# Kernel optimization log

Measured on AMD Instinct MI355X. Metric: run time of the kernel, lower is better.

The kernel has to match this reference:

```python
import jax, jax.numpy as jnp
import numpy as np

N_NODES = 100000
N_EDGES = 600000
DIM = 128          # node feature dim == hidden_dim == output_dim
NUM_HEADS = 4
HEAD_DIM = DIM // NUM_HEADS


def setup_inputs() -> dict:
    key = jax.random.key(0)
    ks = jax.random.split(key, 8)
    s = 1.0 / np.sqrt(DIM).astype(np.float32)
    nodes = jax.random.normal(ks[0], (N_NODES, DIM), jnp.float32)
    senders = jax.random.randint(ks[1], (N_EDGES,), 0, N_NODES, jnp.int32)
    receivers = jax.random.randint(ks[2], (N_EDGES,), 0, N_NODES, jnp.int32)
    Wq = jax.random.normal(ks[3], (DIM, DIM), jnp.float32) * s
    Wk = jax.random.normal(ks[4], (DIM, DIM), jnp.float32) * s
    Wv = jax.random.normal(ks[5], (DIM, DIM), jnp.float32) * s
    Wo = jax.random.normal(ks[6], (DIM, DIM), jnp.float32) * s
    bq = jnp.zeros((DIM,), jnp.float32)
    bk = jnp.zeros((DIM,), jnp.float32)
    bv = jnp.zeros((DIM,), jnp.float32)
    bo = jnp.zeros((DIM,), jnp.float32)
    return {"nodes": nodes, "senders": senders, "receivers": receivers,
            "Wq": Wq, "bq": bq, "Wk": Wk, "bk": bk,
            "Wv": Wv, "bv": bv, "Wo": Wo, "bo": bo}


def reference(nodes, senders, receivers, Wq, bq, Wk, bk, Wv, bv, Wo, bo):
    N = nodes.shape[0]
    inv_sqrt_hd = jnp.float32(1.0 / np.sqrt(HEAD_DIM))
    # Q/K/V projections, reshaped to [N, H, hd]
    q = (nodes @ Wq + bq).reshape(N, NUM_HEADS, HEAD_DIM)
    k = (nodes @ Wk + bk).reshape(N, NUM_HEADS, HEAD_DIM)
    v = (nodes @ Wv + bv).reshape(N, NUM_HEADS, HEAD_DIM)
    # Gather per edge: [E, H, hd]
    q_s = q[senders]
    k_r = k[receivers]
    scores = jnp.sum(q_s * k_r, axis=-1) * inv_sqrt_hd  # [E, H]
    # NOTE: faithful to source -- softmax is over the HEADS axis, not neighbors
    attn = jax.nn.softmax(scores, axis=-1)              # [E, H]
    weighted = (v[senders] * attn[:, :, None]).reshape(-1, DIM)  # [E, DIM]
    aggregated = jax.ops.segment_sum(weighted, receivers, num_segments=N)  # [N, DIM]
    out = aggregated @ Wo + bo
    # residual: nodes.shape[-1] == output_dim
    return out + nodes
```

## Files before the change

### kernel.cpp

```cpp
#include <hip/hip_runtime.h>
#include <hip/hip_bf16.h>

#define N_DIM 128
#define NHEADS 4
#define HEAD_DIM 32

typedef unsigned short bf16_t;
typedef short bf16x8 __attribute__((ext_vector_type(8)));
typedef float f32x4 __attribute__((ext_vector_type(4)));

__device__ __forceinline__ float bf16_to_f32(unsigned int u16) {
    union { unsigned int i; float f; } x;
    x.i = u16 << 16;
    return x.f;
}

__device__ __forceinline__ bf16_t f32_to_bf16(float f) {
    union { float f; unsigned int i; } x;
    x.f = f;
    unsigned int r = x.i + 0x7FFFu + ((x.i >> 16) & 1u);
    return (bf16_t)(r >> 16);
}

#define LDA_STRIDE 136

__global__ __launch_bounds__(128) void transpose_w_kernel(
    const float* __restrict__ Wq, const float* __restrict__ Wk,
    const float* __restrict__ Wv, const float* __restrict__ Wo,
    bf16_t* __restrict__ Wt, bf16_t* __restrict__ Wot)
{
    const int n = blockIdx.x;
    const int k = threadIdx.x;
    const float* W; bf16_t* dst; int nl;
    if (n < 128)      { W = Wq; nl = n;       dst = Wt  + n * 128; }
    else if (n < 256) { W = Wk; nl = n - 128; dst = Wt  + n * 128; }
    else if (n < 384) { W = Wv; nl = n - 256; dst = Wt  + n * 128; }
    else              { W = Wo; nl = n - 384; dst = Wot + (n - 384) * 128; }
    dst[k] = f32_to_bf16(W[k * 128 + nl]);
}

__global__ __launch_bounds__(256) void qkv_mfma_kernel(
    const float* __restrict__ nodes,
    const bf16_t* __restrict__ Wt,
    const float* __restrict__ bq, const float* __restrict__ bk,
    const float* __restrict__ bv,
    bf16_t* __restrict__ qb, bf16_t* __restrict__ kb, bf16_t* __restrict__ vb,
    int N)
{
    __shared__ bf16_t lds_a[32 * LDA_STRIDE];
    const int tid = threadIdx.x;
    const int m0 = blockIdx.x * 32;

#pragma unroll
    for (int i = 0; i < 4; ++i) {
        const int f = tid + 256 * i;
        const int row = f >> 5, c4 = f & 31;
        const int g = m0 + row;
        float4 v = make_float4(0.f, 0.f, 0.f, 0.f);
        if (g < N) v = ((const float4*)nodes)[(size_t)g * 32 + c4];
        ushort4 u;
        u.x = f32_to_bf16(v.x); u.y = f32_to_bf16(v.y);
        u.z = f32_to_bf16(v.z); u.w = f32_to_bf16(v.w);
        *(ushort4*)(lds_a + row * LDA_STRIDE + c4 * 4) = u;
    }
    __syncthreads();

    const int w  = tid >> 6;
    const int l  = tid & 63;
    const int lr = l & 15;
    const int lg = l >> 4;

    bf16x8 a[2][4];
#pragma unroll
    for (int mt = 0; mt < 2; ++mt)
#pragma unroll
        for (int kt = 0; kt < 4; ++kt)
            a[mt][kt] = *(const bf16x8*)(lds_a + (mt * 16 + lr) * LDA_STRIDE
                                         + kt * 32 + lg * 8);

#pragma unroll
    for (int ni = 0; ni < 6; ++ni) {
        const int nt = w * 6 + ni;
        const int col = nt * 16 + lr;
        f32x4 acc0 = {0.f, 0.f, 0.f, 0.f};
        f32x4 acc1 = {0.f, 0.f, 0.f, 0.f};
#pragma unroll
        for (int kt = 0; kt < 4; ++kt) {
            const bf16x8 b = *(const bf16x8*)(Wt + (size_t)col * 128
                                              + kt * 32 + lg * 8);
            acc0 = __builtin_amdgcn_mfma_f32_16x16x32_bf16(a[0][kt], b, acc0, 0, 0, 0);
            acc1 = __builtin_amdgcn_mfma_f32_16x16x32_bf16(a[1][kt], b, acc1, 0, 0, 0);
        }
        bf16_t* dst; int cl; const float* bias;
        if (nt < 8)       { dst = qb; cl = col;       bias = bq; }
        else if (nt < 16) { dst = kb; cl = col - 128; bias = bk; }
        else              { dst = vb; cl = col - 256; bias = bv; }
        const float bb = bias[cl];
#pragma unroll
        for (int j = 0; j < 4; ++j) {
            const int r0 = m0 + lg * 4 + j;
            if (r0 < N) dst[(size_t)r0 * 128 + cl] = f32_to_bf16(acc0[j] + bb);
            const int r1 = m0 + 16 + lg * 4 + j;
            if (r1 < N) dst[(size_t)r1 * 128 + cl] = f32_to_bf16(acc1[j] + bb);
        }
    }
}

__global__ __launch_bounds__(256) void hist_kernel(
    const int* __restrict__ receivers, int* __restrict__ cnt, int E)
{
    const int i = blockIdx.x * 256 + threadIdx.x;
    if (i < E) atomicAdd(&cnt[receivers[i]], 1);
}

__global__ __launch_bounds__(256) void scan_block_kernel(
    const int* __restrict__ cnt, int* __restrict__ starts,
    int* __restrict__ bsum, int N)
{
    __shared__ int sc[256];
    const int t = threadIdx.x;
    const int base = blockIdx.x * 1024 + t * 4;
    int v0 = (base + 0 < N) ? cnt[base + 0] : 0;
    int v1 = (base + 1 < N) ? cnt[base + 1] : 0;
    int v2 = (base + 2 < N) ? cnt[base + 2] : 0;
    int v3 = (base + 3 < N) ? cnt[base + 3] : 0;
    const int s = v0 + v1 + v2 + v3;
    sc[t] = s;
    __syncthreads();
    for (int off = 1; off < 256; off <<= 1) {
        int x = (t >= off) ? sc[t - off] : 0;
        __syncthreads();
        sc[t] += x;
        __syncthreads();
    }
    int excl = sc[t] - s;
    if (base + 0 < N) starts[base + 0] = excl;
    if (base + 1 < N) starts[base + 1] = excl + v0;
    if (base + 2 < N) starts[base + 2] = excl + v0 + v1;
    if (base + 3 < N) starts[base + 3] = excl + v0 + v1 + v2;
    if (t == 255) bsum[blockIdx.x] = sc[255];
}

__global__ __launch_bounds__(256) void scan_top_kernel(
    const int* __restrict__ bsum, int* __restrict__ boff,
    int* __restrict__ starts, int nb, int N)
{
    __shared__ int sc[256];
    const int t = threadIdx.x;
    const int s = (t < nb) ? bsum[t] : 0;
    sc[t] = s;
    __syncthreads();
    for (int off = 1; off < 256; off <<= 1) {
        int x = (t >= off) ? sc[t - off] : 0;
        __syncthreads();
        sc[t] += x;
        __syncthreads();
    }
    if (t < nb) boff[t] = sc[t] - s;
    if (t == 255) starts[N] = sc[255];
}

__global__ __launch_bounds__(256) void scan_add_kernel(
    int* __restrict__ starts, int* __restrict__ cursor,
    const int* __restrict__ boff, int N)
{
    const int t = threadIdx.x;
    const int base = blockIdx.x * 1024 + t * 4;
    const int o = boff[blockIdx.x];
#pragma unroll
    for (int k = 0; k < 4; ++k) {
        const int i = base + k;
        if (i < N) {
            const int v = starts[i] + o;
            starts[i] = v;
            cursor[i] = v;
        }
    }
}

__global__ __launch_bounds__(256) void scatter_kernel(
    const int* __restrict__ senders, const int* __restrict__ receivers,
    int* __restrict__ cursor, int* __restrict__ elist, int E)
{
    const int i = blockIdx.x * 256 + threadIdx.x;
    if (i < E) {
        const int pos = atomicAdd(&cursor[receivers[i]], 1);
        elist[pos] = senders[i];
    }
}

__global__ __launch_bounds__(256) void agg_kernel(
    const int* __restrict__ starts, const int* __restrict__ elist,
    const bf16_t* __restrict__ qb, const bf16_t* __restrict__ kb,
    const bf16_t* __restrict__ vb,
    bf16_t* __restrict__ agg_b, int N)
{
    const int r = blockIdx.x * 4 + (threadIdx.x >> 6);
    const int lane = threadIdx.x & 63;
    if (r >= N) return;

    const int start = starts[r];
    const int end   = starts[r + 1];
    const int c = lane * 2;

    const unsigned int ku = *(const unsigned int*)(kb + (size_t)r * N_DIM + c);
    const float kx = bf16_to_f32(ku & 0xffffu), ky = bf16_to_f32(ku >> 16);

    float ax = 0.f, ay = 0.f;
    const float scale = 0.17677669529663687f;
    const int h = lane >> 4;

    for (int j0 = start; j0 < end; j0 += 64) {
        const int ids = (j0 + lane < end) ? elist[j0 + lane] : 0;
        const int jm = min(64, end - j0);
        for (int j = 0; j < jm; ++j) {
            const int s = __shfl(ids, j);
            const unsigned int qu =
                *(const unsigned int*)(qb + (size_t)s * N_DIM + c);
            const unsigned int vu =
                *(const unsigned int*)(vb + (size_t)s * N_DIM + c);
            const float qx = bf16_to_f32(qu & 0xffffu), qy = bf16_to_f32(qu >> 16);

            float p = qx * kx + qy * ky;
            p += __shfl_xor(p, 1);
            p += __shfl_xor(p, 2);
            p += __shfl_xor(p, 4);
            p += __shfl_xor(p, 8);

            const float s0 = __shfl(p, 0)  * scale;
            const float s1 = __shfl(p, 16) * scale;
            const float s2 = __shfl(p, 32) * scale;
            const float s3 = __shfl(p, 48) * scale;

            const float m = fmaxf(fmaxf(s0, s1), fmaxf(s2, s3));
            const float e0 = __expf(s0 - m);
            const float e1 = __expf(s1 - m);
            const float e2 = __expf(s2 - m);
            const float e3 = __expf(s3 - m);
            const float inv = 1.0f / (e0 + e1 + e2 + e3);
            const float aw = (h == 0 ? e0 : h == 1 ? e1 : h == 2 ? e2 : e3) * inv;

            ax = fmaf(bf16_to_f32(vu & 0xffffu), aw, ax);
            ay = fmaf(bf16_to_f32(vu >> 16),     aw, ay);
        }
    }

    const unsigned int packed =
        (unsigned int)f32_to_bf16(ax) | ((unsigned int)f32_to_bf16(ay) << 16);
    *(unsigned int*)(agg_b + (size_t)r * N_DIM + c) = packed;
}

__global__ __launch_bounds__(256) void out_mfma_b_kernel(
    const float* __restrict__ nodes,
    const bf16_t* __restrict__ agg_b,
    const bf16_t* __restrict__ Wot,
    const float* __restrict__ bo,
    float* __restrict__ out, int N)
{
    __shared__ bf16_t lds_a[32 * LDA_STRIDE];
    const int tid = threadIdx.x;
    const int m0 = blockIdx.x * 32;

#pragma unroll
    for (int i = 0; i < 4; ++i) {
        const int f = tid + 256 * i;
        const int row = f >> 5, c4 = f & 31;
        const int g = m0 + row;
        ushort4 u = make_ushort4(0, 0, 0, 0);
        if (g < N) u = ((const ushort4*)(agg_b + (size_t)g * N_DIM))[c4];
        *(ushort4*)(lds_a + row * LDA_STRIDE + c4 * 4) = u;
    }
    __syncthreads();

    const int w  = tid >> 6;
    const int l  = tid & 63;
    const int lr = l & 15;
    const int lg = l >> 4;

    bf16x8 a[2][4];
#pragma unroll
    for (int mt = 0; mt < 2; ++mt)
#pragma unroll
        for (int kt = 0; kt < 4; ++kt)
            a[mt][kt] = *(const bf16x8*)(lds_a + (mt * 16 + lr) * LDA_STRIDE
                                         + kt * 32 + lg * 8);

#pragma unroll
    for (int ni = 0; ni < 2; ++ni) {
        const int nt = w * 2 + ni;
        const int col = nt * 16 + lr;
        f32x4 acc0 = {0.f, 0.f, 0.f, 0.f};
        f32x4 acc1 = {0.f, 0.f, 0.f, 0.f};
#pragma unroll
        for (int kt = 0; kt < 4; ++kt) {
            const bf16x8 b = *(const bf16x8*)(Wot + (size_t)col * 128
                                              + kt * 32 + lg * 8);
            acc0 = __builtin_amdgcn_mfma_f32_16x16x32_bf16(a[0][kt], b, acc0, 0, 0, 0);
            acc1 = __builtin_amdgcn_mfma_f32_16x16x32_bf16(a[1][kt], b, acc1, 0, 0, 0);
        }
        const float bb = bo[col];
#pragma unroll
        for (int j = 0; j < 4; ++j) {
            const int r0 = m0 + lg * 4 + j;
            if (r0 < N)
                out[(size_t)r0 * 128 + col] =
                    acc0[j] + bb + nodes[(size_t)r0 * 128 + col];
            const int r1 = m0 + 16 + lg * 4 + j;
            if (r1 < N)
                out[(size_t)r1 * 128 + col] =
                    acc1[j] + bb + nodes[(size_t)r1 * 128 + col];
        }
    }
}

__global__ __launch_bounds__(256) void edge_kernel(
    const int* __restrict__ senders, const int* __restrict__ receivers,
    const bf16_t* __restrict__ qb, const bf16_t* __restrict__ kb,
    const bf16_t* __restrict__ vb,
    float* __restrict__ agg, int E)
{
    const int wid = threadIdx.x >> 6;
    const int lane = threadIdx.x & 63;
    const int e = blockIdx.x * 4 + wid;
    if (e >= E) return;

    const int s = senders[e];
    const int r = receivers[e];

    const int c = lane * 2;
    const unsigned int qu = *(const unsigned int*)(qb + (size_t)s * N_DIM + c);
    const unsigned int ku = *(const unsigned int*)(kb + (size_t)r * N_DIM + c);
    const unsigned int vu = *(const unsigned int*)(vb + (size_t)s * N_DIM + c);

    const float qx = bf16_to_f32(qu & 0xffffu), qy = bf16_to_f32(qu >> 16);
    const float kx = bf16_to_f32(ku & 0xffffu), ky = bf16_to_f32(ku >> 16);

    float p = qx * kx + qy * ky;
    p += __shfl_xor(p, 1);
    p += __shfl_xor(p, 2);
    p += __shfl_xor(p, 4);
    p += __shfl_xor(p, 8);

    const float scale = 0.17677669529663687f;
    const float s0 = __shfl(p, 0)  * scale;
    const float s1 = __shfl(p, 16) * scale;
    const float s2 = __shfl(p, 32) * scale;
    const float s3 = __shfl(p, 48) * scale;

    const float m = fmaxf(fmaxf(s0, s1), fmaxf(s2, s3));
    const float e0 = __expf(s0 - m);
    const float e1 = __expf(s1 - m);
    const float e2 = __expf(s2 - m);
    const float e3 = __expf(s3 - m);
    const float inv = 1.0f / (e0 + e1 + e2 + e3);

    const int h = lane >> 4;
    const float aw = (h == 0 ? e0 : h == 1 ? e1 : h == 2 ? e2 : e3) * inv;

    const float wx = bf16_to_f32(vu & 0xffffu) * aw;
    const float wy = bf16_to_f32(vu >> 16) * aw;

    float* dst = agg + (size_t)r * N_DIM + c;
    atomicAdd(dst, wx);
    atomicAdd(dst + 1, wy);
}

__global__ __launch_bounds__(256) void out_mfma_kernel(
    const float* __restrict__ nodes,
    const bf16_t* __restrict__ Wot,
    const float* __restrict__ bo,
    float* __restrict__ out, int N)
{
    __shared__ bf16_t lds_a[32 * LDA_STRIDE];
    const int tid = threadIdx.x;
    const int m0 = blockIdx.x * 32;

#pragma unroll
    for (int i = 0; i < 4; ++i) {
        const int f = tid + 256 * i;
        const int row = f >> 5, c4 = f & 31;
        const int g = m0 + row;
        float4 v = make_float4(0.f, 0.f, 0.f, 0.f);
        if (g < N) v = ((const float4*)out)[(size_t)g * 32 + c4];
        ushort4 u;
        u.x = f32_to_bf16(v.x); u.y = f32_to_bf16(v.y);
        u.z = f32_to_bf16(v.z); u.w = f32_to_bf16(v.w);
        *(ushort4*)(lds_a + row * LDA_STRIDE + c4 * 4) = u;
    }
    __syncthreads();

    const int w  = tid >> 6;
    const int l  = tid & 63;
    const int lr = l & 15;
    const int lg = l >> 4;

    bf16x8 a[2][4];
#pragma unroll
    for (int mt = 0; mt < 2; ++mt)
#pragma unroll
        for (int kt = 0; kt < 4; ++kt)
            a[mt][kt] = *(const bf16x8*)(lds_a + (mt * 16 + lr) * LDA_STRIDE
                                         + kt * 32 + lg * 8);

#pragma unroll
    for (int ni = 0; ni < 2; ++ni) {
        const int nt = w * 2 + ni;
        const int col = nt * 16 + lr;
        f32x4 acc0 = {0.f, 0.f, 0.f, 0.f};
        f32x4 acc1 = {0.f, 0.f, 0.f, 0.f};
#pragma unroll
        for (int kt = 0; kt < 4; ++kt) {
            const bf16x8 b = *(const bf16x8*)(Wot + (size_t)col * 128
                                              + kt * 32 + lg * 8);
            acc0 = __builtin_amdgcn_mfma_f32_16x16x32_bf16(a[0][kt], b, acc0, 0, 0, 0);
            acc1 = __builtin_amdgcn_mfma_f32_16x16x32_bf16(a[1][kt], b, acc1, 0, 0, 0);
        }
        const float bb = bo[col];
#pragma unroll
        for (int j = 0; j < 4; ++j) {
            const int r0 = m0 + lg * 4 + j;
            if (r0 < N)
                out[(size_t)r0 * 128 + col] =
                    acc0[j] + bb + nodes[(size_t)r0 * 128 + col];
            const int r1 = m0 + 16 + lg * 4 + j;
            if (r1 < N)
                out[(size_t)r1 * 128 + col] =
                    acc1[j] + bb + nodes[(size_t)r1 * 128 + col];
        }
    }
}

extern "C" void kernel_launch(void* const* d_in, const int* in_sizes, int n_in,
                              void* d_out, int out_size, void* d_ws, size_t ws_size,
                              hipStream_t stream)
{
    const float* nodes   = (const float*)d_in[0];
    const int* senders   = (const int*)d_in[1];
    const int* receivers = (const int*)d_in[2];
    const float* Wq = (const float*)d_in[3];
    const float* bq = (const float*)d_in[4];
    const float* Wk = (const float*)d_in[5];
    const float* bk = (const float*)d_in[6];
    const float* Wv = (const float*)d_in[7];
    const float* bv = (const float*)d_in[8];
    const float* Wo = (const float*)d_in[9];
    const float* bo = (const float*)d_in[10];

    const int N = in_sizes[0] / N_DIM;
    const int E = in_sizes[1];

    float* out = (float*)d_out;
    char* ws = (char*)d_ws;

    const size_t row_bytes = (size_t)N * N_DIM * sizeof(bf16_t);
    size_t off = 0;
    bf16_t* qb    = (bf16_t*)(ws + off); off += row_bytes;
    bf16_t* kb    = (bf16_t*)(ws + off); off += row_bytes;
    bf16_t* vb    = (bf16_t*)(ws + off); off += row_bytes;
    bf16_t* Wt    = (bf16_t*)(ws + off); off += 384 * 128 * sizeof(bf16_t);
    bf16_t* Wot   = (bf16_t*)(ws + off); off += 128 * 128 * sizeof(bf16_t);
    bf16_t* agg_b = (bf16_t*)(ws + off); off += row_bytes;
    int* cnt      = (int*)(ws + off);    off += (size_t)N * 4;
    int* starts   = (int*)(ws + off);    off += (size_t)(N + 1) * 4;
    int* cursor   = (int*)(ws + off);    off += (size_t)N * 4;
    int* elist    = (int*)(ws + off);    off += (size_t)E * 4;
    int* bsum     = (int*)(ws + off);    off += 256 * 4;
    int* boff     = (int*)(ws + off);    off += 256 * 4;
    const size_t need_csr = off;
    const size_t need_mid = 3 * row_bytes + (384 + 128) * 128 * sizeof(bf16_t);

    const int nb = (N + 1023) / 1024;

    if (ws_size >= need_csr && nb <= 256) {
        transpose_w_kernel<<<512, 128, 0, stream>>>(Wq, Wk, Wv, Wo, Wt, Wot);
        qkv_mfma_kernel<<<(N + 31) / 32, 256, 0, stream>>>(
            nodes, Wt, bq, bk, bv, qb, kb, vb, N);

        hipMemsetAsync(cnt, 0, (size_t)N * 4, stream);
        hist_kernel<<<(E + 255) / 256, 256, 0, stream>>>(receivers, cnt, E);
        scan_block_kernel<<<nb, 256, 0, stream>>>(cnt, starts, bsum, N);
        scan_top_kernel<<<1, 256, 0, stream>>>(bsum, boff, starts, nb, N);
        scan_add_kernel<<<nb, 256, 0, stream>>>(starts, cursor, boff, N);
        scatter_kernel<<<(E + 255) / 256, 256, 0, stream>>>(
            senders, receivers, cursor, elist, E);

        agg_kernel<<<(N + 3) / 4, 256, 0, stream>>>(
            starts, elist, qb, kb, vb, agg_b, N);

        out_mfma_b_kernel<<<(N + 31) / 32, 256, 0, stream>>>(
            nodes, agg_b, Wot, bo, out, N);
    } else if (ws_size >= need_mid) {
        hipMemsetAsync(d_out, 0, (size_t)N * N_DIM * sizeof(float), stream);
        transpose_w_kernel<<<512, 128, 0, stream>>>(Wq, Wk, Wv, Wo, Wt, Wot);
        qkv_mfma_kernel<<<(N + 31) / 32, 256, 0, stream>>>(
            nodes, Wt, bq, bk, bv, qb, kb, vb, N);
        edge_kernel<<<(E + 3) / 4, 256, 0, stream>>>(
            senders, receivers, qb, kb, vb, out, E);
        out_mfma_kernel<<<(N + 31) / 32, 256, 0, stream>>>(
            nodes, Wot, bo, out, N);
    }
}
```

Measured before the change: 356.8 us.

## Precompute per-edge head softmax in separate kernel and permute weights into CSR

Moves the q·k score and head-softmax computation out of the per-receiver aggregation loop into a per-edge kernel that uses one thread per edge and writes packed bf16 attention weights. The scatter kernel now also permutes these weights into CSR order, so the aggregation only gathers v rows and weights. This removes the q gather and the cross-lane shuffle reductions from the inner loop. In exchange it adds an extra kernel with uncoalesced per-thread row reads and extra traffic for the weight buffer, and it rounds the attention weights to bf16.

```diff
diff --git a/kernel.cpp b/kernel.cpp
--- a/kernel.cpp
+++ b/kernel.cpp
@@ -13,6 +13,13 @@
     union { unsigned int i; float f; } x;
     x.i = u16 << 16;
     return x.f;
+}
+
+__device__ __forceinline__ float lof(unsigned int u) {
+    union { unsigned int i; float f; } x; x.i = u << 16; return x.f;
+}
+__device__ __forceinline__ float hif(unsigned int u) {
+    union { unsigned int i; float f; } x; x.i = u & 0xffff0000u; return x.f;
 }
 
 __device__ __forceinline__ bf16_t f32_to_bf16(float f) {
@@ -20,6 +27,12 @@
     x.f = f;
     unsigned int r = x.i + 0x7FFFu + ((x.i >> 16) & 1u);
     return (bf16_t)(r >> 16);
+}
+
+__device__ __forceinline__ float dot2(unsigned int a, unsigned int b, float acc) {
+    acc = fmaf(lof(a), lof(b), acc);
+    acc = fmaf(hif(a), hif(b), acc);
+    return acc;
 }
 
 #define LDA_STRIDE 136
@@ -104,6 +117,44 @@
             if (r1 < N) dst[(size_t)r1 * 128 + cl] = f32_to_bf16(acc1[j] + bb);
         }
     }
+}
+
+__global__ __launch_bounds__(256) void edge_attn_kernel(
+    const int* __restrict__ senders, const int* __restrict__ receivers,
+    const bf16_t* __restrict__ qb, const bf16_t* __restrict__ kb,
+    unsigned int* __restrict__ attn2, int E)
+{
+    const int e = blockIdx.x * 256 + threadIdx.x;
+    if (e >= E) return;
+    const uint4* qr = (const uint4*)(qb + (size_t)senders[e] * N_DIM);
+    const uint4* kr = (const uint4*)(kb + (size_t)receivers[e] * N_DIM);
+
+    float d[4];
+#pragma unroll
+    for (int h = 0; h < 4; ++h) {
+        float acc = 0.f;
+#pragma unroll
+        for (int i = 0; i < 4; ++i) {
+            const uint4 qu = qr[h * 4 + i];
+            const uint4 ku = kr[h * 4 + i];
+            acc = dot2(qu.x, ku.x, acc);
+            acc = dot2(qu.y, ku.y, acc);
+            acc = dot2(qu.z, ku.z, acc);
+            acc = dot2(qu.w, ku.w, acc);
+        }
+        d[h] = acc * 0.17677669529663687f;
+    }
+
+    const float m = fmaxf(fmaxf(d[0], d[1]), fmaxf(d[2], d[3]));
+    float e0 = __expf(d[0] - m), e1 = __expf(d[1] - m);
+    float e2 = __expf(d[2] - m), e3 = __expf(d[3] - m);
+    const float inv = 1.f / (e0 + e1 + e2 + e3);
+    e0 *= inv; e1 *= inv; e2 *= inv; e3 *= inv;
+
+    attn2[(size_t)e * 2 + 0] =
+        (unsigned)f32_to_bf16(e0) | ((unsigned)f32_to_bf16(e1) << 16);
+    attn2[(size_t)e * 2 + 1] =
+        (unsigned)f32_to_bf16(e2) | ((unsigned)f32_to_bf16(e3) << 16);
 }
 
 __global__ __launch_bounds__(256) void hist_kernel(
@@ -180,18 +231,21 @@
 
 __global__ __launch_bounds__(256) void scatter_kernel(
     const int* __restrict__ senders, const int* __restrict__ receivers,
-    int* __restrict__ cursor, int* __restrict__ elist, int E)
+    const unsigned int* __restrict__ attn2,
+    int* __restrict__ cursor, int* __restrict__ elist,
+    unsigned int* __restrict__ wlist2, int E)
 {
     const int i = blockIdx.x * 256 + threadIdx.x;
     if (i < E) {
         const int pos = atomicAdd(&cursor[receivers[i]], 1);
         elist[pos] = senders[i];
-    }
-}
-
-__global__ __launch_bounds__(256) void agg_kernel(
+        ((uint2*)wlist2)[pos] = ((const uint2*)attn2)[i];
+    }
+}
+
+__global__ __launch_bounds__(256) void agg2_kernel(
     const int* __restrict__ starts, const int* __restrict__ elist,
-    const bf16_t* __restrict__ qb, const bf16_t* __restrict__ kb,
+    const unsigned int* __restrict__ wlist2,
     const bf16_t* __restrict__ vb,
     bf16_t* __restrict__ agg_b, int N)
 {
@@ -202,46 +256,23 @@
     const int start = starts[r];
     const int end   = starts[r + 1];
     const int c = lane * 2;
-
-    const unsigned int ku = *(const unsigned int*)(kb + (size_t)r * N_DIM + c);
-    const float kx = bf16_to_f32(ku & 0xffffu), ky = bf16_to_f32(ku >> 16);
+    const int h = lane >> 4;
+    const int hw = h >> 1;
+    const int hs = h & 1;
 
     float ax = 0.f, ay = 0.f;
-    const float scale = 0.17677669529663687f;
-    const int h = lane >> 4;
 
     for (int j0 = start; j0 < end; j0 += 64) {
         const int ids = (j0 + lane < end) ? elist[j0 + lane] : 0;
         const int jm = min(64, end - j0);
         for (int j = 0; j < jm; ++j) {
             const int s = __shfl(ids, j);
-            const unsigned int qu =
-                *(const unsigned int*)(qb + (size_t)s * N_DIM + c);
+            const unsigned int wu = wlist2[(size_t)(j0 + j) * 2 + hw];
+            const float w = hs ? hif(wu) : lof(wu);
             const unsigned int vu =
                 *(const unsigned int*)(vb + (size_t)s * N_DIM + c);
-            const float qx = bf16_to_f32(qu & 0xffffu), qy = bf16_to_f32(qu >> 16);
-
-            float p = qx * kx + qy * ky;
-            p += __shfl_xor(p, 1);
-            p += __shfl_xor(p, 2);
-            p += __shfl_xor(p, 4);
-            p += __shfl_xor(p, 8);
-
-            const float s0 = __shfl(p, 0)  * scale;
-            const float s1 = __shfl(p, 16) * scale;
-            const float s2 = __shfl(p, 32) * scale;
-            const float s3 = __shfl(p, 48) * scale;
-
-            const float m = fmaxf(fmaxf(s0, s1), fmaxf(s2, s3));
-            const float e0 = __expf(s0 - m);
-            const float e1 = __expf(s1 - m);
-            const float e2 = __expf(s2 - m);
-            const float e3 = __expf(s3 - m);
-            const float inv = 1.0f / (e0 + e1 + e2 + e3);
-            const float aw = (h == 0 ? e0 : h == 1 ? e1 : h == 2 ? e2 : e3) * inv;
-
-            ax = fmaf(bf16_to_f32(vu & 0xffffu), aw, ax);
-            ay = fmaf(bf16_to_f32(vu >> 16),     aw, ay);
+            ax = fmaf(lof(vu), w, ax);
+            ay = fmaf(hif(vu), w, ay);
         }
     }
 
@@ -332,8 +363,8 @@
     const unsigned int ku = *(const unsigned int*)(kb + (size_t)r * N_DIM + c);
     const unsigned int vu = *(const unsigned int*)(vb + (size_t)s * N_DIM + c);
 
-    const float qx = bf16_to_f32(qu & 0xffffu), qy = bf16_to_f32(qu >> 16);
-    const float kx = bf16_to_f32(ku & 0xffffu), ky = bf16_to_f32(ku >> 16);
+    const float qx = lof(qu), qy = hif(qu);
+    const float kx = lof(ku), ky = hif(ku);
 
     float p = qx * kx + qy * ky;
     p += __shfl_xor(p, 1);
@@ -357,8 +388,8 @@
     const int h = lane >> 4;
     const float aw = (h == 0 ? e0 : h == 1 ? e1 : h == 2 ? e2 : e3) * inv;
 
-    const float wx = bf16_to_f32(vu & 0xffffu) * aw;
-    const float wy = bf16_to_f32(vu >> 16) * aw;
+    const float wx = lof(vu) * aw;
+    const float wy = hif(vu) * aw;
 
     float* dst = agg + (size_t)r * N_DIM + c;
     atomicAdd(dst, wx);
@@ -464,17 +495,23 @@
     int* starts   = (int*)(ws + off);    off += (size_t)(N + 1) * 4;
     int* cursor   = (int*)(ws + off);    off += (size_t)N * 4;
     int* elist    = (int*)(ws + off);    off += (size_t)E * 4;
+    unsigned int* wlist2 = (unsigned int*)(ws + off); off += (size_t)E * 8;
     int* bsum     = (int*)(ws + off);    off += 256 * 4;
     int* boff     = (int*)(ws + off);    off += 256 * 4;
     const size_t need_csr = off;
     const size_t need_mid = 3 * row_bytes + (384 + 128) * 128 * sizeof(bf16_t);
 
+    unsigned int* attn2 = (unsigned int*)agg_b;
+
     const int nb = (N + 1023) / 1024;
 
     if (ws_size >= need_csr && nb <= 256) {
         transpose_w_kernel<<<512, 128, 0, stream>>>(Wq, Wk, Wv, Wo, Wt, Wot);
         qkv_mfma_kernel<<<(N + 31) / 32, 256, 0, stream>>>(
             nodes, Wt, bq, bk, bv, qb, kb, vb, N);
+
+        edge_attn_kernel<<<(E + 255) / 256, 256, 0, stream>>>(
+            senders, receivers, qb, kb, attn2, E);
 
         hipMemsetAsync(cnt, 0, (size_t)N * 4, stream);
         hist_kernel<<<(E + 255) / 256, 256, 0, stream>>>(receivers, cnt, E);
@@ -482,10 +519,10 @@
         scan_top_kernel<<<1, 256, 0, stream>>>(bsum, boff, starts, nb, N);
         scan_add_kernel<<<nb, 256, 0, stream>>>(starts, cursor, boff, N);
         scatter_kernel<<<(E + 255) / 256, 256, 0, stream>>>(
-            senders, receivers, cursor, elist, E);
-
-        agg_kernel<<<(N + 3) / 4, 256, 0, stream>>>(
-            starts, elist, qb, kb, vb, agg_b, N);
+            senders, receivers, attn2, cursor, elist, wlist2, E);
+
+        agg2_kernel<<<(N + 3) / 4, 256, 0, stream>>>(
+            starts, elist, wlist2, vb, agg_b, N);
 
         out_mfma_b_kernel<<<(N + 31) / 32, 256, 0, stream>>>(
             nodes, agg_b, Wot, bo, out, N);
```

Measured after the change: 394.1 us. 10.5% more time.
